# Kernel optimization log

Hardware: AMD Instinct MI355X
Metric: run time of the kernel (lower is better)

The kernel has to match this reference:

```python
import jax, jax.numpy as jnp
import numpy as np

ALPHA = 0.1
K = 10
N_NODES = 100000
N_EDGES = 3200000


def setup_inputs() -> dict:
    key = jax.random.key(0)
    ks = jax.random.split(key, 8)
    feat = jax.random.normal(ks[0], (N_NODES, 512), dtype=jnp.float32)
    W1 = jax.random.normal(ks[1], (512, 256), dtype=jnp.float32) * (1.0 / np.sqrt(512))
    b1 = jnp.zeros((256,), dtype=jnp.float32)
    W2 = jax.random.normal(ks[2], (256, 64), dtype=jnp.float32) * (1.0 / np.sqrt(256))
    b2 = jnp.zeros((64,), dtype=jnp.float32)
    edge_vals = jax.random.uniform(ks[3], (N_EDGES,), dtype=jnp.float32) / 32.0  # ~row-normalized
    edge_row = jax.random.randint(ks[4], (N_EDGES,), 0, N_NODES, dtype=jnp.int32)
    edge_col = jax.random.randint(ks[5], (N_EDGES,), 0, N_NODES, dtype=jnp.int32)
    return {"features": feat, "W1": W1, "b1": b1, "W2": W2, "b2": b2,
            "edge_vals": edge_vals, "edge_row": edge_row, "edge_col": edge_col}


def _spmm(edge_vals, edge_row, edge_col, x):
    # out[r] = sum_e vals[e] * x[col[e]]  for edges with row[e]==r
    msgs = edge_vals[:, None] * x[edge_col]  # [E, C]
    return jax.ops.segment_sum(msgs, edge_row, num_segments=N_NODES)


def reference(features, W1, b1, W2, b2, edge_vals, edge_row, edge_col):
    # MLP (dropout is identity in eval mode)
    x = jax.nn.relu(features @ W1 + b1)        # [N, nhid]
    x = x @ W2 + b2                             # [N, num_classes]
    h = x
    for _ in range(K):
        x = (1.0 - ALPHA) * _spmm(edge_vals, edge_row, edge_col, x) + ALPHA * h
    return jax.nn.log_softmax(x, axis=1)
```

## Files before the change

kernel.cpp:

```cpp
#include <hip/hip_runtime.h>
#include <hip/hip_bf16.h>
#include <math.h>

#define NNODES 100000
#define NFEAT 512
#define NHID 256
#define NCLS 64
#define ALPHA_C 0.1f
#define NB 4096

typedef short s16x8 __attribute__((ext_vector_type(8)));
typedef float f32x4 __attribute__((ext_vector_type(4)));

__device__ inline unsigned short f2b(float f) {
    union { float f; unsigned u; } v; v.f = f;
    unsigned r = v.u + 0x7fff + ((v.u >> 16) & 1);
    return (unsigned short)(r >> 16);
}
__device__ inline float b2f(unsigned short b) {
    return __uint_as_float((unsigned)b << 16);
}
__device__ inline float blo(unsigned u) { return __uint_as_float(u << 16); }
__device__ inline float bhi(unsigned u) { return __uint_as_float(u & 0xffff0000u); }

__global__ __launch_bounds__(256) void cvtT_kernel(
    const float* __restrict__ src, unsigned short* __restrict__ dst, int R, int Clog2)
{
    int idx = blockIdx.x * 256 + threadIdx.x;
    int C = 1 << Clog2;
    if (idx < R * C) {
        int r = idx >> Clog2, c = idx & (C - 1);
        dst[(size_t)c * R + r] = f2b(src[idx]);
    }
}

#define HID_STRIDE 264

__global__ __launch_bounds__(256) void mlp_mfma_kernel(
    const float* __restrict__ feat, const unsigned short* __restrict__ W1T,
    const float* __restrict__ b1, const unsigned short* __restrict__ W2T,
    const float* __restrict__ b2, unsigned short* __restrict__ h, int N)
{
    __shared__ unsigned short hid_s[64 * HID_STRIDE];
    const int tid  = threadIdx.x;
    const int w    = tid >> 6;
    const int lane = tid & 63;
    const int lr   = lane & 15;
    const int lh   = lane >> 4;
    const int m0   = blockIdx.x * 64;

    f32x4 acc[4][4];
#pragma unroll
    for (int i = 0; i < 4; ++i)
#pragma unroll
        for (int j = 0; j < 4; ++j) acc[i][j] = (f32x4)0.f;

    const float* arow[4];
#pragma unroll
    for (int mi = 0; mi < 4; ++mi) {
        int r = m0 + mi * 16 + lr;
        if (r > N - 1) r = N - 1;
        arow[mi] = feat + (size_t)r * NFEAT;
    }
    const unsigned short* brow[4];
#pragma unroll
    for (int nj = 0; nj < 4; ++nj)
        brow[nj] = W1T + (size_t)(w * 64 + nj * 16 + lr) * NFEAT;

    for (int kb = 0; kb < NFEAT; kb += 32) {
        const int k0 = kb + lh * 8;
        s16x8 afr[4], bfr[4];
#pragma unroll
        for (int mi = 0; mi < 4; ++mi) {
            float4 f0 = *reinterpret_cast<const float4*>(arow[mi] + k0);
            float4 f1 = *reinterpret_cast<const float4*>(arow[mi] + k0 + 4);
            s16x8 a;
            a[0] = f2b(f0.x); a[1] = f2b(f0.y); a[2] = f2b(f0.z); a[3] = f2b(f0.w);
            a[4] = f2b(f1.x); a[5] = f2b(f1.y); a[6] = f2b(f1.z); a[7] = f2b(f1.w);
            afr[mi] = a;
        }
#pragma unroll
        for (int nj = 0; nj < 4; ++nj)
            bfr[nj] = *reinterpret_cast<const s16x8*>(brow[nj] + k0);
#pragma unroll
        for (int mi = 0; mi < 4; ++mi)
#pragma unroll
            for (int nj = 0; nj < 4; ++nj)
                acc[mi][nj] = __builtin_amdgcn_mfma_f32_16x16x32_bf16(
                    afr[mi], bfr[nj], acc[mi][nj], 0, 0, 0);
    }

#pragma unroll
    for (int nj = 0; nj < 4; ++nj) {
        int col = w * 64 + nj * 16 + lr;
        float bias = b1[col];
#pragma unroll
        for (int mi = 0; mi < 4; ++mi)
#pragma unroll
            for (int q = 0; q < 4; ++q) {
                int row = mi * 16 + lh * 4 + q;
                hid_s[row * HID_STRIDE + col] = f2b(fmaxf(acc[mi][nj][q] + bias, 0.f));
            }
    }
    __syncthreads();

    f32x4 acc2[4];
#pragma unroll
    for (int i = 0; i < 4; ++i) acc2[i] = (f32x4)0.f;
    const int cw = w * 16;
    const unsigned short* b2row = W2T + (size_t)(cw + lr) * NHID;
    for (int ks = 0; ks < NHID; ks += 32) {
        int k0 = ks + lh * 8;
        s16x8 bfr = *reinterpret_cast<const s16x8*>(b2row + k0);
#pragma unroll
        for (int mi = 0; mi < 4; ++mi) {
            s16x8 afr = *reinterpret_cast<const s16x8*>(
                &hid_s[(mi * 16 + lr) * HID_STRIDE + k0]);
            acc2[mi] = __builtin_amdgcn_mfma_f32_16x16x32_bf16(afr, bfr, acc2[mi], 0, 0, 0);
        }
    }
    int col = cw + lr;
    float bias2 = b2[col];
#pragma unroll
    for (int mi = 0; mi < 4; ++mi)
#pragma unroll
        for (int q = 0; q < 4; ++q) {
            int row = m0 + mi * 16 + lh * 4 + q;
            if (row < N) h[(size_t)row * NCLS + col] = f2b(acc2[mi][q] + bias2);
        }
}

__global__ __launch_bounds__(256) void hist_kernel(
    const int* __restrict__ row, int* __restrict__ cnt, int E)
{
    int e = blockIdx.x * 256 + threadIdx.x;
    if (e < E) atomicAdd(&cnt[row[e]], 1);
}

__global__ __launch_bounds__(1024) void scanA_kernel(
    const int* __restrict__ cnt, int* __restrict__ excl, int* __restrict__ partials, int n)
{
    __shared__ int wsum[16];
    const int t = threadIdx.x, wid = t >> 6, lane = t & 63;
    const int i = blockIdx.x * 1024 + t;
    int c = (i < n) ? cnt[i] : 0;
    int x = c;
#pragma unroll
    for (int off = 1; off < 64; off <<= 1) {
        int y = __shfl_up(x, off);
        if (lane >= off) x += y;
    }
    if (lane == 63) wsum[wid] = x;
    __syncthreads();
    if (wid == 0 && lane < 16) {
        int wv = wsum[lane];
#pragma unroll
        for (int off = 1; off < 16; off <<= 1) {
            int y = __shfl_up(wv, off);
            if (lane >= off) wv += y;
        }
        wsum[lane] = wv;
    }
    __syncthreads();
    int woff = wid ? wsum[wid - 1] : 0;
    int incl = x + woff;
    if (i < n) excl[i] = incl - c;
    if (t == 1023) partials[blockIdx.x] = incl;
}

__global__ __launch_bounds__(256) void scanB_kernel(
    int* __restrict__ partials, int* __restrict__ row_ptr_end, int nb, int n)
{
    __shared__ int s[256];
    const int t = threadIdx.x;
    int v = (t < nb) ? partials[t] : 0;
    s[t] = v;
    __syncthreads();
    for (int off = 1; off < 256; off <<= 1) {
        int y = (t >= off) ? s[t - off] : 0;
        __syncthreads();
        s[t] += y;
        __syncthreads();
    }
    partials[t] = s[t] - v;
    if (t == 255) row_ptr_end[n] = s[255];
}

__global__ __launch_bounds__(1024) void scanC_kernel(
    int* __restrict__ row_ptr, const int* __restrict__ partials, int n)
{
    const int i = blockIdx.x * 1024 + threadIdx.x;
    if (i < n) row_ptr[i] += partials[blockIdx.x];
}

__global__ __launch_bounds__(256) void binit_kernel(
    const int* __restrict__ row_ptr, int* __restrict__ bcur, int RB, int n)
{
    int b = blockIdx.x * 256 + threadIdx.x;
    if (b < NB) {
        int r = b * RB; if (r > n) r = n;
        bcur[b] = row_ptr[r];
    }
}

__global__ __launch_bounds__(256) void scatterA_kernel(
    const float* __restrict__ vals, const int* __restrict__ row,
    const int* __restrict__ col, int* __restrict__ bcur,
    unsigned long long* __restrict__ stage, int E, int RB)
{
    int e = blockIdx.x * 256 + threadIdx.x;
    if (e < E) {
        int r = row[e];
        int b = r / RB;
        unsigned q = (unsigned)__float2int_rn(vals[e] * 1048576.f);
        if (q > 32767u) q = 32767u;
        unsigned lo = ((unsigned)col[e] << 15) | q;
        int pos = atomicAdd(&bcur[b], 1);
        stage[pos] = ((unsigned long long)(unsigned)r << 32) | lo;
    }
}

__global__ __launch_bounds__(256) void scatterB_kernel(
    const unsigned long long* __restrict__ stage, const int* __restrict__ row_ptr,
    unsigned* __restrict__ ep, int RB, int n)
{
    __shared__ int lcur[64];
    const int b = blockIdx.x;
    const int r0 = b * RB;
    if (r0 >= n) return;
    const int r1 = min(r0 + RB, n);
    const int s0 = row_ptr[r0], s1 = row_ptr[r1];
    for (int i = threadIdx.x; i < r1 - r0; i += 256) lcur[i] = row_ptr[r0 + i];
    __syncthreads();
    for (int i = s0 + threadIdx.x; i < s1; i += 256) {
        unsigned long long rec = stage[i];
        int r = (int)(rec >> 32);
        int p = atomicAdd(&lcur[r - r0], 1);
        ep[p] = (unsigned)rec;
    }
}

__global__ __launch_bounds__(256) void spmm_kernel(
    const unsigned short* __restrict__ x_in, const unsigned short* __restrict__ h,
    unsigned short* __restrict__ x_out, const int* __restrict__ row_ptr,
    const unsigned* __restrict__ ep, int n)
{
    const int wid = threadIdx.x >> 6, lane = threadIdx.x & 63;
    const int r = blockIdx.x * 4 + wid;
    if (r >= n) return;
    const int g  = lane >> 4;
    const int li = lane & 15;
    const int s = row_ptr[r], e_end = row_ptr[r + 1];

    float aA0 = 0.f, aA1 = 0.f, aA2 = 0.f, aA3 = 0.f;
    float aB0 = 0.f, aB1 = 0.f, aB2 = 0.f, aB3 = 0.f;
    int e0 = s;
    for (; e0 + 8 <= e_end; e0 += 8) {
        unsigned p1 = ep[e0 + g];
        unsigned p2 = ep[e0 + 4 + g];
        int   c1 = (int)(p1 >> 15);
        float v1 = (float)(p1 & 0x7fffu) * (1.f / 1048576.f);
        int   c2 = (int)(p2 >> 15);
        float v2 = (float)(p2 & 0x7fffu) * (1.f / 1048576.f);
        uint2 u1 = *reinterpret_cast<const uint2*>(x_in + ((size_t)c1 << 6) + (li << 2));
        uint2 u2 = *reinterpret_cast<const uint2*>(x_in + ((size_t)c2 << 6) + (li << 2));
        aA0 += v1 * blo(u1.x); aA1 += v1 * bhi(u1.x);
        aA2 += v1 * blo(u1.y); aA3 += v1 * bhi(u1.y);
        aB0 += v2 * blo(u2.x); aB1 += v2 * bhi(u2.x);
        aB2 += v2 * blo(u2.y); aB3 += v2 * bhi(u2.y);
    }
    for (; e0 < e_end; e0 += 4) {
        int e = e0 + g;
        if (e < e_end) {
            unsigned p = ep[e];
            int   c = (int)(p >> 15);
            float v = (float)(p & 0x7fffu) * (1.f / 1048576.f);
            uint2 u = *reinterpret_cast<const uint2*>(x_in + ((size_t)c << 6) + (li << 2));
            aA0 += v * blo(u.x); aA1 += v * bhi(u.x);
            aA2 += v * blo(u.y); aA3 += v * bhi(u.y);
        }
    }
    float a0 = aA0 + aB0, a1 = aA1 + aB1, a2 = aA2 + aB2, a3 = aA3 + aB3;
#pragma unroll
    for (int off = 16; off < 64; off <<= 1) {
        a0 += __shfl_xor(a0, off);
        a1 += __shfl_xor(a1, off);
        a2 += __shfl_xor(a2, off);
        a3 += __shfl_xor(a3, off);
    }
    if (g == 0) {
        size_t o = ((size_t)r << 6) + (li << 2);
        uint2 hu = *reinterpret_cast<const uint2*>(h + o);
        float r0 = (1.f - ALPHA_C) * a0 + ALPHA_C * blo(hu.x);
        float r1 = (1.f - ALPHA_C) * a1 + ALPHA_C * bhi(hu.x);
        float r2 = (1.f - ALPHA_C) * a2 + ALPHA_C * blo(hu.y);
        float r3 = (1.f - ALPHA_C) * a3 + ALPHA_C * bhi(hu.y);
        uint2 ou;
        ou.x = ((unsigned)f2b(r1) << 16) | f2b(r0);
        ou.y = ((unsigned)f2b(r3) << 16) | f2b(r2);
        *reinterpret_cast<uint2*>(x_out + o) = ou;
    }
}

__global__ __launch_bounds__(256) void lsm_kernel(
    const unsigned short* __restrict__ x, float* __restrict__ out, int n)
{
    const int wid = threadIdx.x >> 6, lane = threadIdx.x & 63;
    const int r = blockIdx.x * 4 + wid;
    if (r >= n) return;
    float v = b2f(x[(size_t)r * NCLS + lane]);
    float m = v;
#pragma unroll
    for (int o = 32; o > 0; o >>= 1) m = fmaxf(m, __shfl_xor(m, o));
    float ex = expf(v - m);
    float s = ex;
#pragma unroll
    for (int o = 32; o > 0; o >>= 1) s += __shfl_xor(s, o);
    out[(size_t)r * NCLS + lane] = (v - m) - logf(s);
}

extern "C" void kernel_launch(void* const* d_in, const int* in_sizes, int n_in,
                              void* d_out, int out_size, void* d_ws, size_t ws_size,
                              hipStream_t stream)
{
    const float* feat = (const float*)d_in[0];
    const float* W1   = (const float*)d_in[1];
    const float* b1   = (const float*)d_in[2];
    const float* W2   = (const float*)d_in[3];
    const float* b2   = (const float*)d_in[4];
    const float* vals = (const float*)d_in[5];
    const int*   erow = (const int*)d_in[6];
    const int*   ecol = (const int*)d_in[7];
    const int N = in_sizes[0] / NFEAT;
    const int E = in_sizes[5];
    float* out = (float*)d_out;
    const int RB = (N + NB - 1) / NB;

    size_t off = 0;
    auto alloc = [&](size_t bytes) -> void* {
        void* p = (char*)d_ws + off;
        off += (bytes + 255) & ~(size_t)255;
        return p;
    };
    unsigned short*     h        = (unsigned short*)alloc((size_t)N * NCLS * 2);
    unsigned short*     xA       = (unsigned short*)alloc((size_t)N * NCLS * 2);
    unsigned short*     xB       = (unsigned short*)alloc((size_t)N * NCLS * 2);
    int*                row_ptr  = (int*)alloc((size_t)(N + 1) * 4);
    int*                cnt      = (int*)alloc((size_t)N * 4);
    int*                partials = (int*)alloc(256 * 4);
    int*                bcur     = (int*)alloc((size_t)NB * 4);
    unsigned*           ep       = (unsigned*)alloc((size_t)E * 4);
    unsigned long long* stage    = (unsigned long long*)alloc((size_t)E * 8);
    unsigned short*     W1T      = (unsigned short*)alloc((size_t)NHID * NFEAT * 2);
    unsigned short*     W2T      = (unsigned short*)alloc((size_t)NCLS * NHID * 2);
    (void)ws_size;

    cvtT_kernel<<<(NFEAT * NHID + 255) / 256, 256, 0, stream>>>(W1, W1T, NFEAT, 8);
    cvtT_kernel<<<(NHID * NCLS + 255) / 256, 256, 0, stream>>>(W2, W2T, NHID, 6);

    mlp_mfma_kernel<<<(N + 63) / 64, 256, 0, stream>>>(feat, W1T, b1, W2T, b2, h, N);

    hipMemsetAsync(cnt, 0, (size_t)N * 4, stream);
    hist_kernel<<<(E + 255) / 256, 256, 0, stream>>>(erow, cnt, E);
    const int nb = (N + 1023) / 1024;
    scanA_kernel<<<nb, 1024, 0, stream>>>(cnt, row_ptr, partials, N);
    scanB_kernel<<<1, 256, 0, stream>>>(partials, row_ptr, nb, N);
    scanC_kernel<<<nb, 1024, 0, stream>>>(row_ptr, partials, N);
    binit_kernel<<<NB / 256, 256, 0, stream>>>(row_ptr, bcur, RB, N);
    scatterA_kernel<<<(E + 255) / 256, 256, 0, stream>>>(vals, erow, ecol, bcur, stage, E, RB);
    scatterB_kernel<<<NB, 256, 0, stream>>>(stage, row_ptr, ep, RB, N);

    const int gprop = (N + 3) / 4;
    const unsigned short* cur = h;
    for (int i = 0; i < 10; ++i) {
        unsigned short* dst = (i & 1) ? xB : xA;
        spmm_kernel<<<gprop, 256, 0, stream>>>(cur, h, dst, row_ptr, ep, N);
        cur = dst;
    }

    lsm_kernel<<<(N + 3) / 4, 256, 0, stream>>>(cur, out, N);
}
```

Measured before the change: 1.257 ms.

## Replace global-atomic CSR build with two-level bucketed counting sort; unroll SpMM

```diff
diff --git a/kernel.cpp b/kernel.cpp
--- a/kernel.cpp
+++ b/kernel.cpp
@@ -7,7 +7,9 @@
 #define NHID 256
 #define NCLS 64
 #define ALPHA_C 0.1f
-#define NB 4096
+#define NBUCKET 512
+#define NPB 512
+#define RB2 196
 
 typedef short s16x8 __attribute__((ext_vector_type(8)));
 typedef float f32x4 __attribute__((ext_vector_type(4)));
@@ -130,13 +132,6 @@
         }
 }
 
-__global__ __launch_bounds__(256) void hist_kernel(
-    const int* __restrict__ row, int* __restrict__ cnt, int E)
-{
-    int e = blockIdx.x * 256 + threadIdx.x;
-    if (e < E) atomicAdd(&cnt[row[e]], 1);
-}
-
 __global__ __launch_bounds__(1024) void scanA_kernel(
     const int* __restrict__ cnt, int* __restrict__ excl, int* __restrict__ partials, int n)
 {
@@ -169,7 +164,7 @@
 }
 
 __global__ __launch_bounds__(256) void scanB_kernel(
-    int* __restrict__ partials, int* __restrict__ row_ptr_end, int nb, int n)
+    int* __restrict__ partials, int* __restrict__ total_out, int nb, int n)
 {
     __shared__ int s[256];
     const int t = threadIdx.x;
@@ -183,59 +178,86 @@
         __syncthreads();
     }
     partials[t] = s[t] - v;
-    if (t == 255) row_ptr_end[n] = s[255];
+    if (t == 255) total_out[n] = s[255];
 }
 
 __global__ __launch_bounds__(1024) void scanC_kernel(
-    int* __restrict__ row_ptr, const int* __restrict__ partials, int n)
+    int* __restrict__ arr, const int* __restrict__ partials, int n)
 {
     const int i = blockIdx.x * 1024 + threadIdx.x;
-    if (i < n) row_ptr[i] += partials[blockIdx.x];
-}
-
-__global__ __launch_bounds__(256) void binit_kernel(
-    const int* __restrict__ row_ptr, int* __restrict__ bcur, int RB, int n)
-{
-    int b = blockIdx.x * 256 + threadIdx.x;
-    if (b < NB) {
-        int r = b * RB; if (r > n) r = n;
-        bcur[b] = row_ptr[r];
-    }
+    if (i < n) arr[i] += partials[blockIdx.x];
+}
+
+__global__ __launch_bounds__(256) void countP1_kernel(
+    const int* __restrict__ erow, int* __restrict__ cnts, int E, int CE)
+{
+    __shared__ int c[NBUCKET];
+    const int blk = blockIdx.x, t = threadIdx.x;
+    for (int i = t; i < NBUCKET; i += 256) c[i] = 0;
+    __syncthreads();
+    const int e0 = blk * CE, e1 = min(e0 + CE, E);
+    for (int e = e0 + t; e < e1; e += 256)
+        atomicAdd(&c[erow[e] / RB2], 1);
+    __syncthreads();
+    for (int b = t; b < NBUCKET; b += 256)
+        cnts[(size_t)b * NPB + blk] = c[b];
 }
 
 __global__ __launch_bounds__(256) void scatterA_kernel(
-    const float* __restrict__ vals, const int* __restrict__ row,
-    const int* __restrict__ col, int* __restrict__ bcur,
-    unsigned long long* __restrict__ stage, int E, int RB)
-{
-    int e = blockIdx.x * 256 + threadIdx.x;
-    if (e < E) {
-        int r = row[e];
-        int b = r / RB;
+    const float* __restrict__ vals, const int* __restrict__ erow,
+    const int* __restrict__ ecol, const int* __restrict__ S,
+    unsigned long long* __restrict__ stage, int E, int CE)
+{
+    __shared__ int lcur[NBUCKET];
+    const int blk = blockIdx.x, t = threadIdx.x;
+    for (int b = t; b < NBUCKET; b += 256) lcur[b] = S[(size_t)b * NPB + blk];
+    __syncthreads();
+    const int e0 = blk * CE, e1 = min(e0 + CE, E);
+    for (int e = e0 + t; e < e1; e += 256) {
+        int r = erow[e];
         unsigned q = (unsigned)__float2int_rn(vals[e] * 1048576.f);
         if (q > 32767u) q = 32767u;
-        unsigned lo = ((unsigned)col[e] << 15) | q;
-        int pos = atomicAdd(&bcur[b], 1);
+        unsigned lo = ((unsigned)ecol[e] << 15) | q;
+        int pos = atomicAdd(&lcur[r / RB2], 1);
         stage[pos] = ((unsigned long long)(unsigned)r << 32) | lo;
     }
 }
 
 __global__ __launch_bounds__(256) void scatterB_kernel(
-    const unsigned long long* __restrict__ stage, const int* __restrict__ row_ptr,
-    unsigned* __restrict__ ep, int RB, int n)
-{
-    __shared__ int lcur[64];
-    const int b = blockIdx.x;
-    const int r0 = b * RB;
+    const unsigned long long* __restrict__ stage, const int* __restrict__ S,
+    unsigned* __restrict__ ep, int* __restrict__ row_ptr, int n, int E)
+{
+    __shared__ int hcnt[256];
+    __shared__ int lcur[256];
+    const int b = blockIdx.x, t = threadIdx.x;
+    if (b == 0 && t == 0) row_ptr[n] = E;
+    const int r0 = b * RB2;
     if (r0 >= n) return;
-    const int r1 = min(r0 + RB, n);
-    const int s0 = row_ptr[r0], s1 = row_ptr[r1];
-    for (int i = threadIdx.x; i < r1 - r0; i += 256) lcur[i] = row_ptr[r0 + i];
-    __syncthreads();
-    for (int i = s0 + threadIdx.x; i < s1; i += 256) {
+    const int nr = min(RB2, n - r0);
+    const int s0 = S[(size_t)b * NPB];
+    const int s1 = S[(size_t)(b + 1) * NPB];
+    hcnt[t] = 0;
+    __syncthreads();
+    for (int i = s0 + t; i < s1; i += 256)
+        atomicAdd(&hcnt[(int)(stage[i] >> 32) - r0], 1);
+    __syncthreads();
+    int v = hcnt[t];
+    lcur[t] = v;
+    __syncthreads();
+    for (int off = 1; off < 256; off <<= 1) {
+        int y = (t >= off) ? lcur[t - off] : 0;
+        __syncthreads();
+        lcur[t] += y;
+        __syncthreads();
+    }
+    int excl = lcur[t] - v;
+    if (t < nr) row_ptr[r0 + t] = s0 + excl;
+    __syncthreads();
+    lcur[t] = s0 + excl;
+    __syncthreads();
+    for (int i = s0 + t; i < s1; i += 256) {
         unsigned long long rec = stage[i];
-        int r = (int)(rec >> 32);
-        int p = atomicAdd(&lcur[r - r0], 1);
+        int p = atomicAdd(&lcur[(int)(rec >> 32) - r0], 1);
         ep[p] = (unsigned)rec;
     }
 }
@@ -254,25 +276,39 @@
 
     float aA0 = 0.f, aA1 = 0.f, aA2 = 0.f, aA3 = 0.f;
     float aB0 = 0.f, aB1 = 0.f, aB2 = 0.f, aB3 = 0.f;
+    float aC0 = 0.f, aC1 = 0.f, aC2 = 0.f, aC3 = 0.f;
+    float aD0 = 0.f, aD1 = 0.f, aD2 = 0.f, aD3 = 0.f;
     int e0 = s;
-    for (; e0 + 8 <= e_end; e0 += 8) {
-        unsigned p1 = ep[e0 + g];
-        unsigned p2 = ep[e0 + 4 + g];
+    for (; e0 + 16 <= e_end; e0 += 16) {
+        unsigned p1 = __builtin_nontemporal_load(ep + e0 + g);
+        unsigned p2 = __builtin_nontemporal_load(ep + e0 + 4 + g);
+        unsigned p3 = __builtin_nontemporal_load(ep + e0 + 8 + g);
+        unsigned p4 = __builtin_nontemporal_load(ep + e0 + 12 + g);
         int   c1 = (int)(p1 >> 15);
+        int   c2 = (int)(p2 >> 15);
+        int   c3 = (int)(p3 >> 15);
+        int   c4 = (int)(p4 >> 15);
         float v1 = (float)(p1 & 0x7fffu) * (1.f / 1048576.f);
-        int   c2 = (int)(p2 >> 15);
         float v2 = (float)(p2 & 0x7fffu) * (1.f / 1048576.f);
+        float v3 = (float)(p3 & 0x7fffu) * (1.f / 1048576.f);
+        float v4 = (float)(p4 & 0x7fffu) * (1.f / 1048576.f);
         uint2 u1 = *reinterpret_cast<const uint2*>(x_in + ((size_t)c1 << 6) + (li << 2));
         uint2 u2 = *reinterpret_cast<const uint2*>(x_in + ((size_t)c2 << 6) + (li << 2));
+        uint2 u3 = *reinterpret_cast<const uint2*>(x_in + ((size_t)c3 << 6) + (li << 2));
+        uint2 u4 = *reinterpret_cast<const uint2*>(x_in + ((size_t)c4 << 6) + (li << 2));
         aA0 += v1 * blo(u1.x); aA1 += v1 * bhi(u1.x);
         aA2 += v1 * blo(u1.y); aA3 += v1 * bhi(u1.y);
         aB0 += v2 * blo(u2.x); aB1 += v2 * bhi(u2.x);
         aB2 += v2 * blo(u2.y); aB3 += v2 * bhi(u2.y);
+        aC0 += v3 * blo(u3.x); aC1 += v3 * bhi(u3.x);
+        aC2 += v3 * blo(u3.y); aC3 += v3 * bhi(u3.y);
+        aD0 += v4 * blo(u4.x); aD1 += v4 * bhi(u4.x);
+        aD2 += v4 * blo(u4.y); aD3 += v4 * bhi(u4.y);
     }
     for (; e0 < e_end; e0 += 4) {
         int e = e0 + g;
         if (e < e_end) {
-            unsigned p = ep[e];
+            unsigned p = __builtin_nontemporal_load(ep + e);
             int   c = (int)(p >> 15);
             float v = (float)(p & 0x7fffu) * (1.f / 1048576.f);
             uint2 u = *reinterpret_cast<const uint2*>(x_in + ((size_t)c << 6) + (li << 2));
@@ -280,7 +316,10 @@
             aA2 += v * blo(u.y); aA3 += v * bhi(u.y);
         }
     }
-    float a0 = aA0 + aB0, a1 = aA1 + aB1, a2 = aA2 + aB2, a3 = aA3 + aB3;
+    float a0 = (aA0 + aB0) + (aC0 + aD0);
+    float a1 = (aA1 + aB1) + (aC1 + aD1);
+    float a2 = (aA2 + aB2) + (aC2 + aD2);
+    float a3 = (aA3 + aB3) + (aC3 + aD3);
 #pragma unroll
     for (int off = 16; off < 64; off <<= 1) {
         a0 += __shfl_xor(a0, off);
@@ -290,11 +329,13 @@
     }
     if (g == 0) {
         size_t o = ((size_t)r << 6) + (li << 2);
-        uint2 hu = *reinterpret_cast<const uint2*>(h + o);
-        float r0 = (1.f - ALPHA_C) * a0 + ALPHA_C * blo(hu.x);
-        float r1 = (1.f - ALPHA_C) * a1 + ALPHA_C * bhi(hu.x);
-        float r2 = (1.f - ALPHA_C) * a2 + ALPHA_C * blo(hu.y);
-        float r3 = (1.f - ALPHA_C) * a3 + ALPHA_C * bhi(hu.y);
+        const unsigned* hp = reinterpret_cast<const unsigned*>(h + o);
+        unsigned hx = __builtin_nontemporal_load(hp);
+        unsigned hy = __builtin_nontemporal_load(hp + 1);
+        float r0 = (1.f - ALPHA_C) * a0 + ALPHA_C * blo(hx);
+        float r1 = (1.f - ALPHA_C) * a1 + ALPHA_C * bhi(hx);
+        float r2 = (1.f - ALPHA_C) * a2 + ALPHA_C * blo(hy);
+        float r3 = (1.f - ALPHA_C) * a3 + ALPHA_C * bhi(hy);
         uint2 ou;
         ou.x = ((unsigned)f2b(r1) << 16) | f2b(r0);
         ou.y = ((unsigned)f2b(r3) << 16) | f2b(r2);
@@ -334,7 +375,8 @@
     const int N = in_sizes[0] / NFEAT;
     const int E = in_sizes[5];
     float* out = (float*)d_out;
-    const int RB = (N + NB - 1) / NB;
+    const int CE = (E + NPB - 1) / NPB;
+    const int NC = NBUCKET * NPB;
 
     size_t off = 0;
     auto alloc = [&](size_t bytes) -> void* {
@@ -346,9 +388,9 @@
     unsigned short*     xA       = (unsigned short*)alloc((size_t)N * NCLS * 2);
     unsigned short*     xB       = (unsigned short*)alloc((size_t)N * NCLS * 2);
     int*                row_ptr  = (int*)alloc((size_t)(N + 1) * 4);
-    int*                cnt      = (int*)alloc((size_t)N * 4);
+    int*                cnts     = (int*)alloc((size_t)NC * 4);
+    int*                S        = (int*)alloc((size_t)(NC + 1) * 4);
     int*                partials = (int*)alloc(256 * 4);
-    int*                bcur     = (int*)alloc((size_t)NB * 4);
     unsigned*           ep       = (unsigned*)alloc((size_t)E * 4);
     unsigned long long* stage    = (unsigned long long*)alloc((size_t)E * 8);
     unsigned short*     W1T      = (unsigned short*)alloc((size_t)NHID * NFEAT * 2);
@@ -360,15 +402,12 @@
 
     mlp_mfma_kernel<<<(N + 63) / 64, 256, 0, stream>>>(feat, W1T, b1, W2T, b2, h, N);
 
-    hipMemsetAsync(cnt, 0, (size_t)N * 4, stream);
-    hist_kernel<<<(E + 255) / 256, 256, 0, stream>>>(erow, cnt, E);
-    const int nb = (N + 1023) / 1024;
-    scanA_kernel<<<nb, 1024, 0, stream>>>(cnt, row_ptr, partials, N);
-    scanB_kernel<<<1, 256, 0, stream>>>(partials, row_ptr, nb, N);
-    scanC_kernel<<<nb, 1024, 0, stream>>>(row_ptr, partials, N);
-    binit_kernel<<<NB / 256, 256, 0, stream>>>(row_ptr, bcur, RB, N);
-    scatterA_kernel<<<(E + 255) / 256, 256, 0, stream>>>(vals, erow, ecol, bcur, stage, E, RB);
-    scatterB_kernel<<<NB, 256, 0, stream>>>(stage, row_ptr, ep, RB, N);
+    countP1_kernel<<<NPB, 256, 0, stream>>>(erow, cnts, E, CE);
+    scanA_kernel<<<NC / 1024, 1024, 0, stream>>>(cnts, S, partials, NC);
+    scanB_kernel<<<1, 256, 0, stream>>>(partials, S, 256, NC);
+    scanC_kernel<<<NC / 1024, 1024, 0, stream>>>(S, partials, NC);
+    scatterA_kernel<<<NPB, 256, 0, stream>>>(vals, erow, ecol, S, stage, E, CE);
+    scatterB_kernel<<<NBUCKET, 256, 0, stream>>>(stage, S, ep, row_ptr, N, E);
 
     const int gprop = (N + 3) / 4;
     const unsigned short* cur = h;
```

Measured after the change: 1.076 ms. -14.5%, faster.
